# Kernel tuning notes

Hardware: AMD Instinct MI355X
Metric: run time of the kernel (lower is better)

Reference implementation:

```python
import jax, jax.numpy as jnp
import numpy as np

N_NODES = 50000
N_EDGES = 800000
IN_F, HID_F, OUT_F = 256, 128, 64


def setup_inputs() -> dict:
    key = jax.random.key(0)
    ks = jax.random.split(key, 9)
    glorot = lambda k, shp: jax.random.normal(k, shp, jnp.float32) * np.sqrt(2.0 / (shp[0] + shp[1]))
    return {
        "x": jax.random.normal(ks[0], (N_NODES, IN_F), jnp.float32),
        "W1": glorot(ks[1], (IN_F, HID_F)),
        "b1": jnp.zeros((HID_F,), jnp.float32),
        "W2": glorot(ks[2], (HID_F, OUT_F)),
        "b2": jnp.zeros((OUT_F,), jnp.float32),
        "Wf": glorot(ks[3], (OUT_F, 2)),
        "bf": jnp.zeros((2,), jnp.float32),
        "src": jax.random.randint(ks[4], (N_EDGES,), 0, N_NODES, jnp.int32),
        "dst": jax.random.randint(ks[5], (N_EDGES,), 0, N_NODES, jnp.int32),
    }


def _gcn_layer(x, src, dst, W, b):
    # DGL GraphConv, norm='both': h = D_in^{-1/2} A D_out^{-1/2} (x W) + b
    n = x.shape[0]
    ones = jnp.ones((src.shape[0],), x.dtype)
    deg_out = jnp.clip(jax.ops.segment_sum(ones, src, num_segments=n), 1.0)
    deg_in = jnp.clip(jax.ops.segment_sum(ones, dst, num_segments=n), 1.0)
    h = x @ W  # transform first (in_feats >= out_feats), cheaper messages
    h = h * jax.lax.rsqrt(deg_out)[:, None]
    agg = jax.ops.segment_sum(h[src], dst, num_segments=n)  # [N, F] sparse aggregate
    return agg * jax.lax.rsqrt(deg_in)[:, None] + b


def reference(x, W1, b1, W2, b2, Wf, bf, src, dst):
    h1 = jax.nn.relu(_gcn_layer(x, src, dst, W1, b1))
    hidden = _gcn_layer(h1, src, dst, W2, b2)
    logits = hidden @ Wf + bf
    return (logits, hidden)
```

## Files before the change

### kernel.cpp

```cpp
#include <hip/hip_runtime.h>
#include <hip/hip_bf16.h>
#include <cstdint>
#include <cstddef>

#define NNODES 50000
#define NEDGES 800000
#define DHB    64
#define DHC    12500
#define CHUNK1 4096
#define GA1    196
#define GH1TOT (256 * GA1)
#define C2     1000
#define SCB    800
#define GH2TOT (256 * SCB)
#define NBE    ((NEDGES + 255) / 256)

typedef unsigned short u16;
typedef unsigned int u32;
typedef short bfrag8 __attribute__((ext_vector_type(8)));
typedef float f32x4 __attribute__((ext_vector_type(4)));

__device__ __forceinline__ u16 f2bf(float f) {
    union { float f; uint32_t i; } v; v.f = f;
    uint32_t r = (v.i + 0x7FFFu + ((v.i >> 16) & 1u)) >> 16;
    return (u16)r;
}
__device__ __forceinline__ float bflo(u32 p) { union { uint32_t i; float f; } v; v.i = p << 16; return v.f; }
__device__ __forceinline__ float bfhi(u32 p) { union { uint32_t i; float f; } v; v.i = p & 0xFFFF0000u; return v.f; }

__global__ __launch_bounds__(256) void pre_kernel(const float* __restrict__ W1, const float* __restrict__ W2,
                                                  u16* __restrict__ P1, u16* __restrict__ P2,
                                                  const int* __restrict__ src, const int* __restrict__ dst,
                                                  u32* __restrict__ histg, u32* __restrict__ gh1, int nE) {
    __shared__ u32 hh[NNODES / 2];
    int b = blockIdx.x;
    if (b < DHB) {
        for (int j = threadIdx.x; j < NNODES / 2; j += 256) hh[j] = 0;
        __syncthreads();
        int beg = b * DHC, end = min(beg + DHC, nE);
        for (int i = beg + threadIdx.x; i < end; i += 256) {
            u32 n = (u32)src[i];
            atomicAdd(&hh[n >> 1], 1u << ((n & 1) * 16));
        }
        __syncthreads();
        u32* out = histg + (size_t)b * (NNODES / 2);
        for (int j = threadIdx.x; j < NNODES / 2; j += 256) out[j] = hh[j];
    } else if (b < DHB + GA1) {
        int bb = b - DHB;
        hh[threadIdx.x] = 0;
        __syncthreads();
        int beg = bb * CHUNK1, end = min(beg + CHUNK1, nE);
        for (int i = beg + threadIdx.x; i < end; i += 256)
            atomicAdd(&hh[(u32)dst[i] & 255u], 1);
        __syncthreads();
        gh1[threadIdx.x * GA1 + bb] = hh[threadIdx.x];
    } else {
        int i = (b - DHB - GA1) * 256 + threadIdx.x;
        if (i < 256 * 128) {
            int k = i >> 7, n = i & 127;
            P1[((((k >> 3) << 7) + n) << 3) | (k & 7)] = f2bf(W1[i]);
        }
        if (i < 128 * 64) {
            int k = i >> 6, n = i & 63;
            P2[((((k >> 3) << 6) + n) << 3) | (k & 7)] = f2bf(W2[i]);
        }
    }
}

__global__ __launch_bounds__(256) void red_scan1(const u16* __restrict__ histg16, int* __restrict__ deg,
                                                 const u32* __restrict__ gh1, int* __restrict__ scanned,
                                                 int* __restrict__ partials) {
    int i = blockIdx.x * 256 + threadIdx.x;
    if (i < NNODES) {
        int s = 0;
        #pragma unroll 4
        for (int b = 0; b < DHB; b++) s += histg16[(size_t)b * NNODES + i];
        deg[i] = s;
    }
    __shared__ int sd[256];
    int t = threadIdx.x;
    int gi = blockIdx.x * 256 + t;
    int v = (int)gh1[gi];
    sd[t] = v;
    __syncthreads();
    #pragma unroll
    for (int o = 1; o < 256; o <<= 1) {
        int add = (t >= o) ? sd[t - o] : 0;
        __syncthreads();
        sd[t] += add;
        __syncthreads();
    }
    scanned[gi] = sd[t];
    if (t == 255) partials[blockIdx.x] = sd[255];
}

__global__ __launch_bounds__(256) void scatter1(const int* __restrict__ dst, const int* __restrict__ src,
                                                const u32* __restrict__ gh1, const int* __restrict__ scanned,
                                                const int* __restrict__ partials, u32* __restrict__ sbuf, int nE) {
    __shared__ int sd[256];
    __shared__ int offs_l[256];
    __shared__ u32 base[256];
    __shared__ u32 lh[256];
    int t = threadIdx.x;
    int v = (t < GA1) ? partials[t] : 0;
    sd[t] = v;
    __syncthreads();
    #pragma unroll
    for (int o = 1; o < 256; o <<= 1) {
        int add = (t >= o) ? sd[t - o] : 0;
        __syncthreads();
        sd[t] += add;
        __syncthreads();
    }
    offs_l[t] = sd[t] - v;
    __syncthreads();
    int idx = t * GA1 + blockIdx.x;
    base[t] = (u32)(scanned[idx] + offs_l[idx >> 8] - (int)gh1[idx]);
    lh[t] = 0;
    __syncthreads();
    int beg = blockIdx.x * CHUNK1, end = min(beg + CHUNK1, nE);
    for (int i = beg + t; i < end; i += 256) {
        u32 el = ((u32)dst[i] << 16) | (u32)src[i];
        u32 d = (el >> 16) & 255u;
        u32 r = atomicAdd(&lh[d], 1);
        sbuf[base[d] + r] = el;
    }
}

__global__ __launch_bounds__(256) void hist2(const u32* __restrict__ sbuf, u32* __restrict__ gh2, int nE) {
    __shared__ u32 hist[4][256];
    int wave = threadIdx.x >> 6, lane = threadIdx.x & 63;
    int cg = blockIdx.x * 4 + wave;
    for (int j = lane; j < 256; j += 64) hist[wave][j] = 0;
    __syncthreads();
    int beg = cg * C2, end = min(beg + C2, nE);
    for (int i = beg + lane; i < end; i += 64)
        atomicAdd(&hist[wave][sbuf[i] >> 24], 1);
    __syncthreads();
    for (int j = lane; j < 256; j += 64)
        gh2[j * SCB + cg] = hist[wave][j];
}

__global__ __launch_bounds__(256) void scan2(const u32* __restrict__ gh2, int* __restrict__ scanned,
                                             int* __restrict__ partials) {
    __shared__ int sd[256];
    int t = threadIdx.x;
    int gi = blockIdx.x * 256 + t;
    int v = (int)gh2[gi];
    sd[t] = v;
    __syncthreads();
    #pragma unroll
    for (int o = 1; o < 256; o <<= 1) {
        int add = (t >= o) ? sd[t - o] : 0;
        __syncthreads();
        sd[t] += add;
        __syncthreads();
    }
    scanned[gi] = sd[t];
    if (t == 255) partials[blockIdx.x] = sd[255];
}

__global__ __launch_bounds__(256) void scatter2_stable(const u32* __restrict__ sbuf, const u32* __restrict__ gh2,
                                                       const int* __restrict__ scanned, const int* __restrict__ partials,
                                                       u32* __restrict__ sorted, int nE) {
    __shared__ int sd[256];
    __shared__ int offs_l[800];
    __shared__ u32 run[4][256];
    int t = threadIdx.x;
    int v[4]; int s = 0;
    #pragma unroll
    for (int j = 0; j < 4; j++) { int idx = t * 4 + j; v[j] = (idx < 800) ? partials[idx] : 0; s += v[j]; }
    sd[t] = s;
    __syncthreads();
    #pragma unroll
    for (int o = 1; o < 256; o <<= 1) {
        int add = (t >= o) ? sd[t - o] : 0;
        __syncthreads();
        sd[t] += add;
        __syncthreads();
    }
    int bse = sd[t] - s;
    #pragma unroll
    for (int j = 0; j < 4; j++) { int idx = t * 4 + j; if (idx < 800) offs_l[idx] = bse; bse += v[j]; }
    __syncthreads();
    int wave = t >> 6, lane = t & 63;
    int cg = blockIdx.x * 4 + wave;
    for (int j = lane; j < 256; j += 64) {
        int idx = j * SCB + cg;
        run[wave][j] = (u32)(scanned[idx] + offs_l[idx >> 8] - (int)gh2[idx]);
    }
    __syncthreads();
    int beg = cg * C2, end = min(beg + C2, nE);
    for (int i0 = beg; i0 < end; i0 += 64) {
        int i = i0 + lane;
        int active = (i < end);
        u32 el = active ? sbuf[i] : 0;
        u32 d = el >> 24;
        unsigned long long m = __ballot(active);
        #pragma unroll
        for (int b = 0; b < 8; b++) {
            unsigned long long bb_ = __ballot(active && ((d >> b) & 1));
            m &= ((d >> b) & 1) ? bb_ : ~bb_;
        }
        if (active) {
            int lanerank = __popcll(m & ((1ull << lane) - 1ull));
            int leader = __ffsll((long long)m) - 1;
            u32 base = 0;
            if (lane == leader) base = atomicAdd(&run[wave][d], (u32)__popcll(m));
            base = (u32)__shfl((int)base, leader, 64);
            sorted[base + (u32)lanerank] = el;
        }
    }
}

__global__ __launch_bounds__(256) void bounds_kernel(const u32* __restrict__ sorted, int* __restrict__ rp, int nE) {
    int e = blockIdx.x * 256 + threadIdx.x;
    if (e >= nE) return;
    int k = (int)(sorted[e] >> 16);
    int kp = e ? (int)(sorted[e - 1] >> 16) : -1;
    if (k != kp)
        for (int n = kp + 1; n <= k; n++) rp[n] = e;
    if (e == nE - 1)
        for (int n = k + 1; n <= NNODES; n++) rp[n] = nE;
}


template <int K, int N, bool AF32>
__global__ __launch_bounds__(256) void gemm_scaled(const void* __restrict__ A_, const u16* __restrict__ Wp,
                                                   const int* __restrict__ deg, u16* __restrict__ out, int M) {
    const int lane = threadIdx.x & 63;
    const int wave = threadIdx.x >> 6;
    const int m = lane & 15;
    const int q = lane >> 4;
    const int row0 = blockIdx.x * 64 + wave * 16;

    int rowa = row0 + m; if (rowa > M - 1) rowa = M - 1;

    constexpr int NT = N / 16;
    f32x4 acc[NT];
    #pragma unroll
    for (int t = 0; t < NT; t++) acc[t] = (f32x4){0.f, 0.f, 0.f, 0.f};

    #pragma unroll
    for (int kc = 0; kc < K; kc += 32) {
        bfrag8 af;
        if constexpr (AF32) {
            const float* ap = (const float*)A_ + (size_t)rowa * K + q * 8 + kc;
            const float4 x0 = *(const float4*)(ap);
            const float4 x1 = *(const float4*)(ap + 4);
            af[0] = (short)f2bf(x0.x); af[1] = (short)f2bf(x0.y);
            af[2] = (short)f2bf(x0.z); af[3] = (short)f2bf(x0.w);
            af[4] = (short)f2bf(x1.x); af[5] = (short)f2bf(x1.y);
            af[6] = (short)f2bf(x1.z); af[7] = (short)f2bf(x1.w);
        } else {
            const u16* ap = (const u16*)A_ + (size_t)rowa * K + q * 8 + kc;
            af = *(const bfrag8*)ap;
        }
        const u16* bbase = Wp + ((size_t)(((kc >> 3) + q) * N) + m) * 8;
        #pragma unroll
        for (int t = 0; t < NT; t++) {
            bfrag8 bf_ = *(const bfrag8*)(bbase + t * 128);
            acc[t] = __builtin_amdgcn_mfma_f32_16x16x32_bf16(af, bf_, acc[t], 0, 0, 0);
        }
    }
    #pragma unroll
    for (int r = 0; r < 4; r++) {
        int gr = row0 + q * 4 + r;
        if (gr < M) {
            int dO = deg[gr]; if (dO < 1) dO = 1;
            float s = rsqrtf((float)dO);
            #pragma unroll
            for (int t = 0; t < NT; t++)
                out[(size_t)gr * N + t * 16 + m] = f2bf(acc[t][r] * s);
        }
    }
}

__global__ __launch_bounds__(256) void gather1(const uint4* __restrict__ h,
                                               const int* __restrict__ row_ptr,
                                               const u32* __restrict__ sorted, const float* __restrict__ b1,
                                               uint4* __restrict__ h1out, int nNodes) {
    int node = (blockIdx.x * 256 + threadIdx.x) >> 4;
    int l = threadIdx.x & 15;
    if (node >= nNodes) return;
    int beg = row_ptr[node], end = row_ptr[node + 1];
    float a[8] = {0.f, 0.f, 0.f, 0.f, 0.f, 0.f, 0.f, 0.f};
    for (int e = beg; e < end; e += 4) {
        uint4 p[4];
        #pragma unroll
        for (int j = 0; j < 4; j++) {
            int ee = e + j; ee = (ee < end - 1) ? ee : end - 1;
            p[j] = h[(size_t)(sorted[ee] & 0xFFFFu) * 16 + l];
        }
        #pragma unroll
        for (int j = 0; j < 4; j++)
            if (e + j < end) {
                a[0] += bflo(p[j].x); a[1] += bfhi(p[j].x);
                a[2] += bflo(p[j].y); a[3] += bfhi(p[j].y);
                a[4] += bflo(p[j].z); a[5] += bfhi(p[j].z);
                a[6] += bflo(p[j].w); a[7] += bfhi(p[j].w);
            }
    }
    int dI = end - beg; if (dI < 1) dI = 1;
    float r = rsqrtf((float)dI);
    const float4 bA = *(const float4*)(b1 + 8 * l);
    const float4 bB = *(const float4*)(b1 + 8 * l + 4);
    float v0 = fmaxf(a[0] * r + bA.x, 0.f), v1 = fmaxf(a[1] * r + bA.y, 0.f);
    float v2 = fmaxf(a[2] * r + bA.z, 0.f), v3 = fmaxf(a[3] * r + bA.w, 0.f);
    float v4 = fmaxf(a[4] * r + bB.x, 0.f), v5 = fmaxf(a[5] * r + bB.y, 0.f);
    float v6 = fmaxf(a[6] * r + bB.z, 0.f), v7 = fmaxf(a[7] * r + bB.w, 0.f);
    uint4 o;
    o.x = ((u32)f2bf(v1) << 16) | f2bf(v0);
    o.y = ((u32)f2bf(v3) << 16) | f2bf(v2);
    o.z = ((u32)f2bf(v5) << 16) | f2bf(v4);
    o.w = ((u32)f2bf(v7) << 16) | f2bf(v6);
    h1out[(size_t)node * 16 + l] = o;
}

__global__ __launch_bounds__(256) void gather2(const uint4* __restrict__ h2,
                                               const int* __restrict__ row_ptr,
                                               const u32* __restrict__ sorted, const float* __restrict__ b2,
                                               const float* __restrict__ Wf, const float* __restrict__ bfv,
                                               float* __restrict__ logits, float* __restrict__ hidden, int nNodes) {
    int node = (blockIdx.x * 256 + threadIdx.x) >> 3;
    int l = threadIdx.x & 7;
    if (node >= nNodes) return;
    int beg = row_ptr[node], end = row_ptr[node + 1];
    float a[8] = {0.f, 0.f, 0.f, 0.f, 0.f, 0.f, 0.f, 0.f};
    for (int e = beg; e < end; e += 4) {
        uint4 p[4];
        #pragma unroll
        for (int j = 0; j < 4; j++) {
            int ee = e + j; ee = (ee < end - 1) ? ee : end - 1;
            p[j] = h2[(size_t)(sorted[ee] & 0xFFFFu) * 8 + l];
        }
        #pragma unroll
        for (int j = 0; j < 4; j++)
            if (e + j < end) {
                a[0] += bflo(p[j].x); a[1] += bfhi(p[j].x);
                a[2] += bflo(p[j].y); a[3] += bfhi(p[j].y);
                a[4] += bflo(p[j].z); a[5] += bfhi(p[j].z);
                a[6] += bflo(p[j].w); a[7] += bfhi(p[j].w);
            }
    }
    int dI = end - beg; if (dI < 1) dI = 1;
    float r = rsqrtf((float)dI);
    float v[8];
    #pragma unroll
    for (int f = 0; f < 8; f++) v[f] = a[f] * r + b2[8 * l + f];
    float4 oA = {v[0], v[1], v[2], v[3]};
    float4 oB = {v[4], v[5], v[6], v[7]};
    ((float4*)hidden)[(size_t)node * 16 + 2 * l + 0] = oA;
    ((float4*)hidden)[(size_t)node * 16 + 2 * l + 1] = oB;
    float l0 = 0.f, l1 = 0.f;
    #pragma unroll
    for (int f = 0; f < 8; f++) {
        l0 += v[f] * Wf[(8 * l + f) * 2 + 0];
        l1 += v[f] * Wf[(8 * l + f) * 2 + 1];
    }
    #pragma unroll
    for (int off = 4; off > 0; off >>= 1) {
        l0 += __shfl_down(l0, off, 8);
        l1 += __shfl_down(l1, off, 8);
    }
    if (l == 0) {
        logits[(size_t)node * 2 + 0] = l0 + bfv[0];
        logits[(size_t)node * 2 + 1] = l1 + bfv[1];
    }
}

extern "C" void kernel_launch(void* const* d_in, const int* in_sizes, int n_in,
                              void* d_out, int out_size, void* d_ws, size_t ws_size,
                              hipStream_t stream) {
    const float* x   = (const float*)d_in[0];
    const float* W1  = (const float*)d_in[1];
    const float* b1  = (const float*)d_in[2];
    const float* W2  = (const float*)d_in[3];
    const float* b2  = (const float*)d_in[4];
    const float* Wf  = (const float*)d_in[5];
    const float* bfv = (const float*)d_in[6];
    const int* src = (const int*)d_in[7];
    const int* dst = (const int*)d_in[8];

    float* out_logits = (float*)d_out;
    float* out_hidden = (float*)d_out + 2 * NNODES;

    char* ws = (char*)d_ws;
    size_t off = 0;
    auto alloc = [&](size_t bytes) { void* p = ws + off; off += (bytes + 255) & ~(size_t)255; return p; };
    u32*   gh1     = (u32*)alloc(GH1TOT * 4);
    u32*   gh2     = (u32*)alloc(GH2TOT * 4);
    int*   scanned = (int*)alloc(GH2TOT * 4);
    int*   partials= (int*)alloc(1024 * 4);
    u32*   sbuf    = (u32*)alloc((size_t)NEDGES * 4);
    u32*   sorted  = (u32*)alloc((size_t)NEDGES * 4);
    u32*   histg   = (u32*)alloc((size_t)DHB * (NNODES / 2) * 4);
    int*   deg_out = (int*)alloc(NNODES * 4);
    int*   row_ptr = (int*)alloc((NNODES + 1) * 4);
    u16*   Wp1     = (u16*)alloc(256 * 128 * 2);
    u16*   Wp2     = (u16*)alloc(128 * 64 * 2);
    u16*   h       = (u16*)alloc((size_t)NNODES * 128 * 2);
    u16*   h1      = (u16*)alloc((size_t)NNODES * 128 * 2);
    u16*   h2      = (u16*)alloc((size_t)NNODES * 64 * 2);

    pre_kernel<<<DHB + GA1 + 128, 256, 0, stream>>>(W1, W2, Wp1, Wp2, src, dst, histg, gh1, NEDGES);
    red_scan1<<<GA1, 256, 0, stream>>>((const u16*)histg, deg_out, gh1, scanned, partials);
    scatter1<<<GA1, 256, 0, stream>>>(dst, src, gh1, scanned, partials, sbuf, NEDGES);
    hist2<<<SCB / 4, 256, 0, stream>>>(sbuf, gh2, NEDGES);
    scan2<<<GH2TOT / 256, 256, 0, stream>>>(gh2, scanned, partials);
    scatter2_stable<<<SCB / 4, 256, 0, stream>>>(sbuf, gh2, scanned, partials, sorted, NEDGES);
    bounds_kernel<<<NBE, 256, 0, stream>>>(sorted, row_ptr, NEDGES);
    gemm_scaled<256, 128, true><<<(NNODES + 63) / 64, 256, 0, stream>>>(x, Wp1, deg_out, h, NNODES);
    gather1<<<(NNODES * 16 + 255) / 256, 256, 0, stream>>>((const uint4*)h, row_ptr, sorted, b1,
                                                           (uint4*)h1, NNODES);
    gemm_scaled<128, 64, false><<<(NNODES + 63) / 64, 256, 0, stream>>>(h1, Wp2, deg_out, h2, NNODES);
    gather2<<<(NNODES * 8 + 255) / 256, 256, 0, stream>>>((const uint4*)h2, row_ptr, sorted, b2, Wf, bfv,
                                                          out_logits, out_hidden, NNODES);
}
```

Before: 234.3 us.

## Fuse graph-building kernels into one cooperative kernel with grid syncs

The degree histogram, two-pass radix sort by destination, scans and row-pointer construction were seven separate kernel launches. They are merged into a single cooperative kernel of 256 blocks that uses grid.sync() between phases, with chunk sizes retuned to fit the fixed grid. This removes per-launch overhead and the gaps between small dependent kernels. In exchange, each phase is limited to 256 blocks with large shared memory, which lowers parallelism and occupancy, and grid-wide barriers have their own cost.

New measurement: 444.5 us. +89.7%, slower.

```diff
diff --git a/kernel.cpp b/kernel.cpp
--- a/kernel.cpp
+++ b/kernel.cpp
@@ -1,19 +1,22 @@
 #include <hip/hip_runtime.h>
 #include <hip/hip_bf16.h>
+#include <hip/hip_cooperative_groups.h>
 #include <cstdint>
 #include <cstddef>
 
+namespace cg = cooperative_groups;
+
 #define NNODES 50000
 #define NEDGES 800000
+#define NB     256
 #define DHB    64
 #define DHC    12500
-#define CHUNK1 4096
-#define GA1    196
+#define GA1    192
+#define CHUNK1 4167
 #define GH1TOT (256 * GA1)
-#define C2     1000
-#define SCB    800
-#define GH2TOT (256 * SCB)
-#define NBE    ((NEDGES + 255) / 256)
+#define SCB2   1024
+#define C2     782
+#define GH2TOT (256 * SCB2)
 
 typedef unsigned short u16;
 typedef unsigned int u32;
@@ -28,200 +31,206 @@
 __device__ __forceinline__ float bflo(u32 p) { union { uint32_t i; float f; } v; v.i = p << 16; return v.f; }
 __device__ __forceinline__ float bfhi(u32 p) { union { uint32_t i; float f; } v; v.i = p & 0xFFFF0000u; return v.f; }
 
-__global__ __launch_bounds__(256) void pre_kernel(const float* __restrict__ W1, const float* __restrict__ W2,
-                                                  u16* __restrict__ P1, u16* __restrict__ P2,
-                                                  const int* __restrict__ src, const int* __restrict__ dst,
-                                                  u32* __restrict__ histg, u32* __restrict__ gh1, int nE) {
-    __shared__ u32 hh[NNODES / 2];
-    int b = blockIdx.x;
+__global__ void build_graph(const float* __restrict__ W1, const float* __restrict__ W2,
+                            u16* __restrict__ P1w, u16* __restrict__ P2w,
+                            const int* __restrict__ src, const int* __restrict__ dst,
+                            u32* __restrict__ histg, u32* __restrict__ gh1,
+                            int* __restrict__ scan1, int* __restrict__ part1,
+                            u32* __restrict__ sbuf, u32* __restrict__ gh2,
+                            int* __restrict__ scan2g, int* __restrict__ part2,
+                            u32* __restrict__ sorted, int* __restrict__ deg,
+                            int* __restrict__ rp, int nE) {
+    __shared__ __align__(16) u32 ls[25088];
+    cg::grid_group grid = cg::this_grid();
+    const int b = blockIdx.x, t = threadIdx.x;
+
     if (b < DHB) {
-        for (int j = threadIdx.x; j < NNODES / 2; j += 256) hh[j] = 0;
+        for (int j = t; j < NNODES / 2; j += 256) ls[j] = 0;
         __syncthreads();
         int beg = b * DHC, end = min(beg + DHC, nE);
-        for (int i = beg + threadIdx.x; i < end; i += 256) {
+        for (int i = beg + t; i < end; i += 256) {
             u32 n = (u32)src[i];
-            atomicAdd(&hh[n >> 1], 1u << ((n & 1) * 16));
+            atomicAdd(&ls[n >> 1], 1u << ((n & 1) * 16));
         }
         __syncthreads();
         u32* out = histg + (size_t)b * (NNODES / 2);
-        for (int j = threadIdx.x; j < NNODES / 2; j += 256) out[j] = hh[j];
-    } else if (b < DHB + GA1) {
-        int bb = b - DHB;
-        hh[threadIdx.x] = 0;
-        __syncthreads();
-        int beg = bb * CHUNK1, end = min(beg + CHUNK1, nE);
-        for (int i = beg + threadIdx.x; i < end; i += 256)
-            atomicAdd(&hh[(u32)dst[i] & 255u], 1);
-        __syncthreads();
-        gh1[threadIdx.x * GA1 + bb] = hh[threadIdx.x];
+        for (int j = t; j < NNODES / 2; j += 256) out[j] = ls[j];
     } else {
-        int i = (b - DHB - GA1) * 256 + threadIdx.x;
-        if (i < 256 * 128) {
+        int c = b - DHB;
+        ls[t] = 0;
+        __syncthreads();
+        int beg = c * CHUNK1, end = min(beg + CHUNK1, nE);
+        for (int i = beg + t; i < end; i += 256)
+            atomicAdd(&ls[(u32)dst[i] & 255u], 1);
+        __syncthreads();
+        gh1[t * GA1 + c] = ls[t];
+        if (b < 192) {
+            int i = (b - 64) * 256 + t;
             int k = i >> 7, n = i & 127;
-            P1[((((k >> 3) << 7) + n) << 3) | (k & 7)] = f2bf(W1[i]);
-        }
-        if (i < 128 * 64) {
+            P1w[((((k >> 3) << 7) + n) << 3) | (k & 7)] = f2bf(W1[i]);
+        } else if (b < 224) {
+            int i = (b - 192) * 256 + t;
             int k = i >> 6, n = i & 63;
-            P2[((((k >> 3) << 6) + n) << 3) | (k & 7)] = f2bf(W2[i]);
-        }
-    }
-}
-
-__global__ __launch_bounds__(256) void red_scan1(const u16* __restrict__ histg16, int* __restrict__ deg,
-                                                 const u32* __restrict__ gh1, int* __restrict__ scanned,
-                                                 int* __restrict__ partials) {
-    int i = blockIdx.x * 256 + threadIdx.x;
-    if (i < NNODES) {
-        int s = 0;
-        #pragma unroll 4
-        for (int b = 0; b < DHB; b++) s += histg16[(size_t)b * NNODES + i];
-        deg[i] = s;
-    }
-    __shared__ int sd[256];
-    int t = threadIdx.x;
-    int gi = blockIdx.x * 256 + t;
-    int v = (int)gh1[gi];
-    sd[t] = v;
-    __syncthreads();
-    #pragma unroll
-    for (int o = 1; o < 256; o <<= 1) {
-        int add = (t >= o) ? sd[t - o] : 0;
-        __syncthreads();
-        sd[t] += add;
-        __syncthreads();
-    }
-    scanned[gi] = sd[t];
-    if (t == 255) partials[blockIdx.x] = sd[255];
-}
-
-__global__ __launch_bounds__(256) void scatter1(const int* __restrict__ dst, const int* __restrict__ src,
-                                                const u32* __restrict__ gh1, const int* __restrict__ scanned,
-                                                const int* __restrict__ partials, u32* __restrict__ sbuf, int nE) {
-    __shared__ int sd[256];
-    __shared__ int offs_l[256];
-    __shared__ u32 base[256];
-    __shared__ u32 lh[256];
-    int t = threadIdx.x;
-    int v = (t < GA1) ? partials[t] : 0;
-    sd[t] = v;
-    __syncthreads();
-    #pragma unroll
-    for (int o = 1; o < 256; o <<= 1) {
-        int add = (t >= o) ? sd[t - o] : 0;
-        __syncthreads();
-        sd[t] += add;
-        __syncthreads();
-    }
-    offs_l[t] = sd[t] - v;
-    __syncthreads();
-    int idx = t * GA1 + blockIdx.x;
-    base[t] = (u32)(scanned[idx] + offs_l[idx >> 8] - (int)gh1[idx]);
-    lh[t] = 0;
-    __syncthreads();
-    int beg = blockIdx.x * CHUNK1, end = min(beg + CHUNK1, nE);
-    for (int i = beg + t; i < end; i += 256) {
-        u32 el = ((u32)dst[i] << 16) | (u32)src[i];
-        u32 d = (el >> 16) & 255u;
-        u32 r = atomicAdd(&lh[d], 1);
-        sbuf[base[d] + r] = el;
-    }
-}
-
-__global__ __launch_bounds__(256) void hist2(const u32* __restrict__ sbuf, u32* __restrict__ gh2, int nE) {
-    __shared__ u32 hist[4][256];
-    int wave = threadIdx.x >> 6, lane = threadIdx.x & 63;
-    int cg = blockIdx.x * 4 + wave;
-    for (int j = lane; j < 256; j += 64) hist[wave][j] = 0;
-    __syncthreads();
-    int beg = cg * C2, end = min(beg + C2, nE);
-    for (int i = beg + lane; i < end; i += 64)
-        atomicAdd(&hist[wave][sbuf[i] >> 24], 1);
-    __syncthreads();
-    for (int j = lane; j < 256; j += 64)
-        gh2[j * SCB + cg] = hist[wave][j];
-}
-
-__global__ __launch_bounds__(256) void scan2(const u32* __restrict__ gh2, int* __restrict__ scanned,
-                                             int* __restrict__ partials) {
-    __shared__ int sd[256];
-    int t = threadIdx.x;
-    int gi = blockIdx.x * 256 + t;
-    int v = (int)gh2[gi];
-    sd[t] = v;
-    __syncthreads();
-    #pragma unroll
-    for (int o = 1; o < 256; o <<= 1) {
-        int add = (t >= o) ? sd[t - o] : 0;
-        __syncthreads();
-        sd[t] += add;
-        __syncthreads();
-    }
-    scanned[gi] = sd[t];
-    if (t == 255) partials[blockIdx.x] = sd[255];
-}
-
-__global__ __launch_bounds__(256) void scatter2_stable(const u32* __restrict__ sbuf, const u32* __restrict__ gh2,
-                                                       const int* __restrict__ scanned, const int* __restrict__ partials,
-                                                       u32* __restrict__ sorted, int nE) {
-    __shared__ int sd[256];
-    __shared__ int offs_l[800];
-    __shared__ u32 run[4][256];
-    int t = threadIdx.x;
-    int v[4]; int s = 0;
-    #pragma unroll
-    for (int j = 0; j < 4; j++) { int idx = t * 4 + j; v[j] = (idx < 800) ? partials[idx] : 0; s += v[j]; }
-    sd[t] = s;
-    __syncthreads();
-    #pragma unroll
-    for (int o = 1; o < 256; o <<= 1) {
-        int add = (t >= o) ? sd[t - o] : 0;
-        __syncthreads();
-        sd[t] += add;
-        __syncthreads();
-    }
-    int bse = sd[t] - s;
-    #pragma unroll
-    for (int j = 0; j < 4; j++) { int idx = t * 4 + j; if (idx < 800) offs_l[idx] = bse; bse += v[j]; }
-    __syncthreads();
-    int wave = t >> 6, lane = t & 63;
-    int cg = blockIdx.x * 4 + wave;
-    for (int j = lane; j < 256; j += 64) {
-        int idx = j * SCB + cg;
-        run[wave][j] = (u32)(scanned[idx] + offs_l[idx >> 8] - (int)gh2[idx]);
-    }
-    __syncthreads();
-    int beg = cg * C2, end = min(beg + C2, nE);
-    for (int i0 = beg; i0 < end; i0 += 64) {
-        int i = i0 + lane;
-        int active = (i < end);
-        u32 el = active ? sbuf[i] : 0;
-        u32 d = el >> 24;
-        unsigned long long m = __ballot(active);
-        #pragma unroll
-        for (int b = 0; b < 8; b++) {
-            unsigned long long bb_ = __ballot(active && ((d >> b) & 1));
-            m &= ((d >> b) & 1) ? bb_ : ~bb_;
-        }
-        if (active) {
-            int lanerank = __popcll(m & ((1ull << lane) - 1ull));
-            int leader = __ffsll((long long)m) - 1;
-            u32 base = 0;
-            if (lane == leader) base = atomicAdd(&run[wave][d], (u32)__popcll(m));
-            base = (u32)__shfl((int)base, leader, 64);
-            sorted[base + (u32)lanerank] = el;
-        }
-    }
-}
-
-__global__ __launch_bounds__(256) void bounds_kernel(const u32* __restrict__ sorted, int* __restrict__ rp, int nE) {
-    int e = blockIdx.x * 256 + threadIdx.x;
-    if (e >= nE) return;
-    int k = (int)(sorted[e] >> 16);
-    int kp = e ? (int)(sorted[e - 1] >> 16) : -1;
-    if (k != kp)
-        for (int n = kp + 1; n <= k; n++) rp[n] = e;
-    if (e == nE - 1)
-        for (int n = k + 1; n <= NNODES; n++) rp[n] = nE;
+            P2w[((((k >> 3) << 6) + n) << 3) | (k & 7)] = f2bf(W2[i]);
+        }
+    }
+    grid.sync();
+
+    if (b < GA1) {
+        int* sd = (int*)ls;
+        int gi = b * 256 + t;
+        int v = (int)gh1[gi];
+        sd[t] = v;
+        __syncthreads();
+        #pragma unroll
+        for (int o = 1; o < 256; o <<= 1) {
+            int add = (t >= o) ? sd[t - o] : 0;
+            __syncthreads();
+            sd[t] += add;
+            __syncthreads();
+        }
+        scan1[gi] = sd[t];
+        if (t == 255) part1[b] = sd[255];
+    }
+    {
+        int n = b * 196 + t;
+        if (t < 196 && n < NNODES) {
+            int s = 0;
+            #pragma unroll 4
+            for (int bb = 0; bb < DHB; bb++)
+                s += (int)((histg[(size_t)bb * (NNODES / 2) + (n >> 1)] >> ((n & 1) * 16)) & 0xFFFFu);
+            deg[n] = s;
+        }
+    }
+    grid.sync();
+
+    if (b >= DHB) {
+        int c = b - DHB;
+        int* sd    = (int*)ls;
+        int* offsL = (int*)(ls + 256);
+        u32* baseL = ls + 512;
+        u32* lh    = ls + 768;
+        int v = (t < GA1) ? part1[t] : 0;
+        sd[t] = v;
+        __syncthreads();
+        #pragma unroll
+        for (int o = 1; o < 256; o <<= 1) {
+            int add = (t >= o) ? sd[t - o] : 0;
+            __syncthreads();
+            sd[t] += add;
+            __syncthreads();
+        }
+        if (t < GA1) offsL[t] = sd[t] - v;
+        __syncthreads();
+        int idx = t * GA1 + c;
+        baseL[t] = (u32)(scan1[idx] + offsL[idx >> 8] - (int)gh1[idx]);
+        lh[t] = 0;
+        __syncthreads();
+        int beg = c * CHUNK1, end = min(beg + CHUNK1, nE);
+        for (int i = beg + t; i < end; i += 256) {
+            u32 el = ((u32)dst[i] << 16) | (u32)src[i];
+            u32 d = (el >> 16) & 255u;
+            u32 r = atomicAdd(&lh[d], 1);
+            sbuf[baseL[d] + r] = el;
+        }
+    }
+    grid.sync();
+
+    {
+        int w = t >> 6, lane = t & 63;
+        int cgi = b * 4 + w;
+        for (int j = lane; j < 256; j += 64) ls[w * 256 + j] = 0;
+        __syncthreads();
+        int beg = cgi * C2, end = min(beg + C2, nE);
+        for (int i = beg + lane; i < end; i += 64)
+            atomicAdd(&ls[w * 256 + (sbuf[i] >> 24)], 1);
+        __syncthreads();
+        for (int j = lane; j < 256; j += 64)
+            gh2[j * SCB2 + cgi] = ls[w * 256 + j];
+    }
+    grid.sync();
+
+    {
+        int* sd = (int*)ls;
+        for (int gg = 0; gg < 4; gg++) {
+            int g = b * 4 + gg;
+            int gi = g * 256 + t;
+            int v = (int)gh2[gi];
+            sd[t] = v;
+            __syncthreads();
+            #pragma unroll
+            for (int o = 1; o < 256; o <<= 1) {
+                int add = (t >= o) ? sd[t - o] : 0;
+                __syncthreads();
+                sd[t] += add;
+                __syncthreads();
+            }
+            scan2g[gi] = sd[t];
+            if (t == 255) part2[g] = sd[255];
+            __syncthreads();
+        }
+    }
+    grid.sync();
+
+    {
+        int* sd    = (int*)ls;
+        int* offs2 = (int*)(ls + 256);
+        u32* run   = ls + 1280;
+        int v4[4]; int s = 0;
+        #pragma unroll
+        for (int j = 0; j < 4; j++) { v4[j] = part2[t * 4 + j]; s += v4[j]; }
+        sd[t] = s;
+        __syncthreads();
+        #pragma unroll
+        for (int o = 1; o < 256; o <<= 1) {
+            int add = (t >= o) ? sd[t - o] : 0;
+            __syncthreads();
+            sd[t] += add;
+            __syncthreads();
+        }
+        int bse = sd[t] - s;
+        #pragma unroll
+        for (int j = 0; j < 4; j++) { offs2[t * 4 + j] = bse; bse += v4[j]; }
+        __syncthreads();
+        int w = t >> 6, lane = t & 63;
+        int cgi = b * 4 + w;
+        for (int j = lane; j < 256; j += 64) {
+            int idx = j * SCB2 + cgi;
+            run[w * 256 + j] = (u32)(scan2g[idx] + offs2[idx >> 8] - (int)gh2[idx]);
+        }
+        __syncthreads();
+        int beg = cgi * C2, end = min(beg + C2, nE);
+        for (int i0 = beg; i0 < end; i0 += 64) {
+            int i = i0 + lane;
+            int active = (i < end);
+            u32 el = active ? sbuf[i] : 0;
+            u32 d = el >> 24;
+            unsigned long long m = __ballot(active);
+            #pragma unroll
+            for (int bb = 0; bb < 8; bb++) {
+                unsigned long long bm = __ballot(active && ((d >> bb) & 1));
+                m &= ((d >> bb) & 1) ? bm : ~bm;
+            }
+            if (active) {
+                int lanerank = __popcll(m & ((1ull << lane) - 1ull));
+                int leader = __ffsll((long long)m) - 1;
+                u32 base = 0;
+                if (lane == leader) base = atomicAdd(&run[w * 256 + d], (u32)__popcll(m));
+                base = (u32)__shfl((int)base, leader, 64);
+                sorted[base + (u32)lanerank] = el;
+            }
+        }
+    }
+    grid.sync();
+
+    for (int e = b * 256 + t; e < nE; e += NB * 256) {
+        int k = (int)(sorted[e] >> 16);
+        int kp = e ? (int)(sorted[e - 1] >> 16) : -1;
+        if (k != kp)
+            for (int n = kp + 1; n <= k; n++) rp[n] = e;
+        if (e == nE - 1)
+            for (int n = k + 1; n <= NNODES; n++) rp[n] = nE;
+    }
 }
 
 
@@ -276,8 +285,7 @@
     }
 }
 
-__global__ __launch_bounds__(256) void gather1(const uint4* __restrict__ h,
-                                               const int* __restrict__ row_ptr,
+__global__ __launch_bounds__(256) void gather1(const uint4* __restrict__ h, const int* __restrict__ row_ptr,
                                                const u32* __restrict__ sorted, const float* __restrict__ b1,
                                                uint4* __restrict__ h1out, int nNodes) {
     int node = (blockIdx.x * 256 + threadIdx.x) >> 4;
@@ -317,8 +325,7 @@
     h1out[(size_t)node * 16 + l] = o;
 }
 
-__global__ __launch_bounds__(256) void gather2(const uint4* __restrict__ h2,
-                                               const int* __restrict__ row_ptr,
+__global__ __launch_bounds__(256) void gather2(const uint4* __restrict__ h2, const int* __restrict__ row_ptr,
                                                const u32* __restrict__ sorted, const float* __restrict__ b2,
                                                const float* __restrict__ Wf, const float* __restrict__ bfv,
                                                float* __restrict__ logits, float* __restrict__ hidden, int nNodes) {
@@ -390,8 +397,10 @@
     auto alloc = [&](size_t bytes) { void* p = ws + off; off += (bytes + 255) & ~(size_t)255; return p; };
     u32*   gh1     = (u32*)alloc(GH1TOT * 4);
     u32*   gh2     = (u32*)alloc(GH2TOT * 4);
-    int*   scanned = (int*)alloc(GH2TOT * 4);
-    int*   partials= (int*)alloc(1024 * 4);
+    int*   scan1   = (int*)alloc(GH1TOT * 4);
+    int*   scan2g  = (int*)alloc(GH2TOT * 4);
+    int*   part1   = (int*)alloc(256 * 4);
+    int*   part2   = (int*)alloc(1024 * 4);
     u32*   sbuf    = (u32*)alloc((size_t)NEDGES * 4);
     u32*   sorted  = (u32*)alloc((size_t)NEDGES * 4);
     u32*   histg   = (u32*)alloc((size_t)DHB * (NNODES / 2) * 4);
@@ -403,13 +412,13 @@
     u16*   h1      = (u16*)alloc((size_t)NNODES * 128 * 2);
     u16*   h2      = (u16*)alloc((size_t)NNODES * 64 * 2);
 
-    pre_kernel<<<DHB + GA1 + 128, 256, 0, stream>>>(W1, W2, Wp1, Wp2, src, dst, histg, gh1, NEDGES);
-    red_scan1<<<GA1, 256, 0, stream>>>((const u16*)histg, deg_out, gh1, scanned, partials);
-    scatter1<<<GA1, 256, 0, stream>>>(dst, src, gh1, scanned, partials, sbuf, NEDGES);
-    hist2<<<SCB / 4, 256, 0, stream>>>(sbuf, gh2, NEDGES);
-    scan2<<<GH2TOT / 256, 256, 0, stream>>>(gh2, scanned, partials);
-    scatter2_stable<<<SCB / 4, 256, 0, stream>>>(sbuf, gh2, scanned, partials, sorted, NEDGES);
-    bounds_kernel<<<NBE, 256, 0, stream>>>(sorted, row_ptr, NEDGES);
+    int nE = NEDGES;
+    void* kargs[] = { (void*)&W1, (void*)&W2, (void*)&Wp1, (void*)&Wp2, (void*)&src, (void*)&dst,
+                      (void*)&histg, (void*)&gh1, (void*)&scan1, (void*)&part1, (void*)&sbuf,
+                      (void*)&gh2, (void*)&scan2g, (void*)&part2, (void*)&sorted,
+                      (void*)&deg_out, (void*)&row_ptr, (void*)&nE };
+    hipLaunchCooperativeKernel((void*)build_graph, dim3(NB), dim3(256), kargs, 0, stream);
+
     gemm_scaled<256, 128, true><<<(NNODES + 63) / 64, 256, 0, stream>>>(x, Wp1, deg_out, h, NNODES);
     gather1<<<(NNODES * 16 + 255) / 256, 256, 0, stream>>>((const uint4*)h, row_ptr, sorted, b1,
                                                            (uint4*)h1, NNODES);
```

## Replace two-pass LSD radix sort with MSD bucket partition plus per-bucket local sort

Applied to the files above, without the earlier changes.

The edge sort by destination switches from a low-byte-then-high-byte LSD radix (hist2, scan2, a stable ballot scatter, and a bounds kernel) to an MSD scheme. Edges are first partitioned by dst>>8 into 196 buckets over 256 chunks. Each bucket is then sorted by the low byte in a single block that also writes row_ptr directly. This removes three kernel launches and a full pass over the edges. Order within a node becomes nondeterministic because of the atomics, so float summation order can vary between runs. The gather loops also unroll to 8 loads in flight.

Result: faster. 217.2 us (-7.3%).

```diff
diff --git a/kernel.cpp b/kernel.cpp
--- a/kernel.cpp
+++ b/kernel.cpp
@@ -7,13 +7,9 @@
 #define NEDGES 800000
 #define DHB    64
 #define DHC    12500
-#define CHUNK1 4096
-#define GA1    196
-#define GH1TOT (256 * GA1)
-#define C2     1000
-#define SCB    800
-#define GH2TOT (256 * SCB)
-#define NBE    ((NEDGES + 255) / 256)
+#define NCH    256
+#define CHUNK1 3125
+#define NBUCK  196
 
 typedef unsigned short u16;
 typedef unsigned int u32;
@@ -33,29 +29,29 @@
                                                   const int* __restrict__ src, const int* __restrict__ dst,
                                                   u32* __restrict__ histg, u32* __restrict__ gh1, int nE) {
     __shared__ u32 hh[NNODES / 2];
-    int b = blockIdx.x;
+    int b = blockIdx.x, t = threadIdx.x;
     if (b < DHB) {
-        for (int j = threadIdx.x; j < NNODES / 2; j += 256) hh[j] = 0;
+        for (int j = t; j < NNODES / 2; j += 256) hh[j] = 0;
         __syncthreads();
         int beg = b * DHC, end = min(beg + DHC, nE);
-        for (int i = beg + threadIdx.x; i < end; i += 256) {
+        for (int i = beg + t; i < end; i += 256) {
             u32 n = (u32)src[i];
             atomicAdd(&hh[n >> 1], 1u << ((n & 1) * 16));
         }
         __syncthreads();
         u32* out = histg + (size_t)b * (NNODES / 2);
-        for (int j = threadIdx.x; j < NNODES / 2; j += 256) out[j] = hh[j];
-    } else if (b < DHB + GA1) {
-        int bb = b - DHB;
-        hh[threadIdx.x] = 0;
-        __syncthreads();
-        int beg = bb * CHUNK1, end = min(beg + CHUNK1, nE);
-        for (int i = beg + threadIdx.x; i < end; i += 256)
-            atomicAdd(&hh[(u32)dst[i] & 255u], 1);
-        __syncthreads();
-        gh1[threadIdx.x * GA1 + bb] = hh[threadIdx.x];
+        for (int j = t; j < NNODES / 2; j += 256) out[j] = hh[j];
+    } else if (b < DHB + NCH) {
+        int c = b - DHB;
+        hh[t] = 0;
+        __syncthreads();
+        int beg = c * CHUNK1, end = min(beg + CHUNK1, nE);
+        for (int i = beg + t; i < end; i += 256)
+            atomicAdd(&hh[(u32)dst[i] >> 8], 1);
+        __syncthreads();
+        gh1[t * NCH + c] = hh[t];
     } else {
-        int i = (b - DHB - GA1) * 256 + threadIdx.x;
+        int i = (b - DHB - NCH) * 256 + t;
         if (i < 256 * 128) {
             int k = i >> 7, n = i & 127;
             P1[((((k >> 3) << 7) + n) << 3) | (k & 7)] = f2bf(W1[i]);
@@ -67,19 +63,20 @@
     }
 }
 
-__global__ __launch_bounds__(256) void red_scan1(const u16* __restrict__ histg16, int* __restrict__ deg,
-                                                 const u32* __restrict__ gh1, int* __restrict__ scanned,
-                                                 int* __restrict__ partials) {
-    int i = blockIdx.x * 256 + threadIdx.x;
-    if (i < NNODES) {
+__global__ __launch_bounds__(256) void red_scan1(const u32* __restrict__ histg, int* __restrict__ deg,
+                                                 const u32* __restrict__ gh1, int* __restrict__ scan1,
+                                                 int* __restrict__ part1) {
+    int t = threadIdx.x, b = blockIdx.x;
+    int n = b * 196 + t;
+    if (t < 196 && n < NNODES) {
         int s = 0;
         #pragma unroll 4
-        for (int b = 0; b < DHB; b++) s += histg16[(size_t)b * NNODES + i];
-        deg[i] = s;
+        for (int bb = 0; bb < DHB; bb++)
+            s += (int)((histg[(size_t)bb * (NNODES / 2) + (n >> 1)] >> ((n & 1) * 16)) & 0xFFFFu);
+        deg[n] = s;
     }
     __shared__ int sd[256];
-    int t = threadIdx.x;
-    int gi = blockIdx.x * 256 + t;
+    int gi = b * NCH + t;
     int v = (int)gh1[gi];
     sd[t] = v;
     __syncthreads();
@@ -90,19 +87,19 @@
         sd[t] += add;
         __syncthreads();
     }
-    scanned[gi] = sd[t];
-    if (t == 255) partials[blockIdx.x] = sd[255];
+    scan1[gi] = sd[t];
+    if (t == 255) part1[b] = sd[255];
 }
 
 __global__ __launch_bounds__(256) void scatter1(const int* __restrict__ dst, const int* __restrict__ src,
-                                                const u32* __restrict__ gh1, const int* __restrict__ scanned,
-                                                const int* __restrict__ partials, u32* __restrict__ sbuf, int nE) {
+                                                const u32* __restrict__ gh1, const int* __restrict__ scan1,
+                                                const int* __restrict__ part1, u32* __restrict__ sbuf, int nE) {
     __shared__ int sd[256];
-    __shared__ int offs_l[256];
+    __shared__ int offs[256];
     __shared__ u32 base[256];
     __shared__ u32 lh[256];
-    int t = threadIdx.x;
-    int v = (t < GA1) ? partials[t] : 0;
+    int t = threadIdx.x, c = blockIdx.x;
+    int v = part1[t];
     sd[t] = v;
     __syncthreads();
     #pragma unroll
@@ -112,41 +109,27 @@
         sd[t] += add;
         __syncthreads();
     }
-    offs_l[t] = sd[t] - v;
-    __syncthreads();
-    int idx = t * GA1 + blockIdx.x;
-    base[t] = (u32)(scanned[idx] + offs_l[idx >> 8] - (int)gh1[idx]);
+    offs[t] = sd[t] - v;
+    __syncthreads();
+    base[t] = (u32)(scan1[t * NCH + c] + offs[t] - (int)gh1[t * NCH + c]);
     lh[t] = 0;
     __syncthreads();
-    int beg = blockIdx.x * CHUNK1, end = min(beg + CHUNK1, nE);
+    int beg = c * CHUNK1, end = min(beg + CHUNK1, nE);
     for (int i = beg + t; i < end; i += 256) {
         u32 el = ((u32)dst[i] << 16) | (u32)src[i];
-        u32 d = (el >> 16) & 255u;
+        u32 d = el >> 24;
         u32 r = atomicAdd(&lh[d], 1);
         sbuf[base[d] + r] = el;
     }
 }
 
-__global__ __launch_bounds__(256) void hist2(const u32* __restrict__ sbuf, u32* __restrict__ gh2, int nE) {
-    __shared__ u32 hist[4][256];
-    int wave = threadIdx.x >> 6, lane = threadIdx.x & 63;
-    int cg = blockIdx.x * 4 + wave;
-    for (int j = lane; j < 256; j += 64) hist[wave][j] = 0;
-    __syncthreads();
-    int beg = cg * C2, end = min(beg + C2, nE);
-    for (int i = beg + lane; i < end; i += 64)
-        atomicAdd(&hist[wave][sbuf[i] >> 24], 1);
-    __syncthreads();
-    for (int j = lane; j < 256; j += 64)
-        gh2[j * SCB + cg] = hist[wave][j];
-}
-
-__global__ __launch_bounds__(256) void scan2(const u32* __restrict__ gh2, int* __restrict__ scanned,
-                                             int* __restrict__ partials) {
+__global__ __launch_bounds__(256) void sort_bucket(const u32* __restrict__ sbuf, const int* __restrict__ part1,
+                                                   u32* __restrict__ sorted, int* __restrict__ rp, int nE) {
     __shared__ int sd[256];
-    int t = threadIdx.x;
-    int gi = blockIdx.x * 256 + t;
-    int v = (int)gh2[gi];
+    __shared__ int cnt[256];
+    __shared__ int cursor[256];
+    int t = threadIdx.x, b = blockIdx.x;
+    int v = part1[t];
     sd[t] = v;
     __syncthreads();
     #pragma unroll
@@ -156,21 +139,17 @@
         sd[t] += add;
         __syncthreads();
     }
-    scanned[gi] = sd[t];
-    if (t == 255) partials[blockIdx.x] = sd[255];
-}
-
-__global__ __launch_bounds__(256) void scatter2_stable(const u32* __restrict__ sbuf, const u32* __restrict__ gh2,
-                                                       const int* __restrict__ scanned, const int* __restrict__ partials,
-                                                       u32* __restrict__ sorted, int nE) {
-    __shared__ int sd[256];
-    __shared__ int offs_l[800];
-    __shared__ u32 run[4][256];
-    int t = threadIdx.x;
-    int v[4]; int s = 0;
-    #pragma unroll
-    for (int j = 0; j < 4; j++) { int idx = t * 4 + j; v[j] = (idx < 800) ? partials[idx] : 0; s += v[j]; }
-    sd[t] = s;
+    __shared__ int bs_s, bl_s;
+    if (t == b) { bs_s = sd[t] - v; bl_s = v; }
+    __syncthreads();
+    int bstart = bs_s, bend = bstart + bl_s;
+    cnt[t] = 0;
+    __syncthreads();
+    for (int i = bstart + t; i < bend; i += 256)
+        atomicAdd(&cnt[(sbuf[i] >> 16) & 255u], 1);
+    __syncthreads();
+    int cv = cnt[t];
+    sd[t] = cv;
     __syncthreads();
     #pragma unroll
     for (int o = 1; o < 256; o <<= 1) {
@@ -179,49 +158,17 @@
         sd[t] += add;
         __syncthreads();
     }
-    int bse = sd[t] - s;
-    #pragma unroll
-    for (int j = 0; j < 4; j++) { int idx = t * 4 + j; if (idx < 800) offs_l[idx] = bse; bse += v[j]; }
-    __syncthreads();
-    int wave = t >> 6, lane = t & 63;
-    int cg = blockIdx.x * 4 + wave;
-    for (int j = lane; j < 256; j += 64) {
-        int idx = j * SCB + cg;
-        run[wave][j] = (u32)(scanned[idx] + offs_l[idx >> 8] - (int)gh2[idx]);
-    }
-    __syncthreads();
-    int beg = cg * C2, end = min(beg + C2, nE);
-    for (int i0 = beg; i0 < end; i0 += 64) {
-        int i = i0 + lane;
-        int active = (i < end);
-        u32 el = active ? sbuf[i] : 0;
-        u32 d = el >> 24;
-        unsigned long long m = __ballot(active);
-        #pragma unroll
-        for (int b = 0; b < 8; b++) {
-            unsigned long long bb_ = __ballot(active && ((d >> b) & 1));
-            m &= ((d >> b) & 1) ? bb_ : ~bb_;
-        }
-        if (active) {
-            int lanerank = __popcll(m & ((1ull << lane) - 1ull));
-            int leader = __ffsll((long long)m) - 1;
-            u32 base = 0;
-            if (lane == leader) base = atomicAdd(&run[wave][d], (u32)__popcll(m));
-            base = (u32)__shfl((int)base, leader, 64);
-            sorted[base + (u32)lanerank] = el;
-        }
-    }
-}
-
-__global__ __launch_bounds__(256) void bounds_kernel(const u32* __restrict__ sorted, int* __restrict__ rp, int nE) {
-    int e = blockIdx.x * 256 + threadIdx.x;
-    if (e >= nE) return;
-    int k = (int)(sorted[e] >> 16);
-    int kp = e ? (int)(sorted[e - 1] >> 16) : -1;
-    if (k != kp)
-        for (int n = kp + 1; n <= k; n++) rp[n] = e;
-    if (e == nE - 1)
-        for (int n = k + 1; n <= NNODES; n++) rp[n] = nE;
+    int excl = sd[t] - cv;
+    int node = b * 256 + t;
+    if (node < NNODES) rp[node] = bstart + excl;
+    if (b == NBUCK - 1 && t == 0) rp[NNODES] = nE;
+    cursor[t] = excl;
+    __syncthreads();
+    for (int i = bstart + t; i < bend; i += 256) {
+        u32 el = sbuf[i];
+        int r = atomicAdd(&cursor[(el >> 16) & 255u], 1);
+        sorted[bstart + r] = el;
+    }
 }
 
 
@@ -276,8 +223,7 @@
     }
 }
 
-__global__ __launch_bounds__(256) void gather1(const uint4* __restrict__ h,
-                                               const int* __restrict__ row_ptr,
+__global__ __launch_bounds__(256) void gather1(const uint4* __restrict__ h, const int* __restrict__ row_ptr,
                                                const u32* __restrict__ sorted, const float* __restrict__ b1,
                                                uint4* __restrict__ h1out, int nNodes) {
     int node = (blockIdx.x * 256 + threadIdx.x) >> 4;
@@ -285,15 +231,15 @@
     if (node >= nNodes) return;
     int beg = row_ptr[node], end = row_ptr[node + 1];
     float a[8] = {0.f, 0.f, 0.f, 0.f, 0.f, 0.f, 0.f, 0.f};
-    for (int e = beg; e < end; e += 4) {
-        uint4 p[4];
-        #pragma unroll
-        for (int j = 0; j < 4; j++) {
+    for (int e = beg; e < end; e += 8) {
+        uint4 p[8];
+        #pragma unroll
+        for (int j = 0; j < 8; j++) {
             int ee = e + j; ee = (ee < end - 1) ? ee : end - 1;
             p[j] = h[(size_t)(sorted[ee] & 0xFFFFu) * 16 + l];
         }
         #pragma unroll
-        for (int j = 0; j < 4; j++)
+        for (int j = 0; j < 8; j++)
             if (e + j < end) {
                 a[0] += bflo(p[j].x); a[1] += bfhi(p[j].x);
                 a[2] += bflo(p[j].y); a[3] += bfhi(p[j].y);
@@ -317,8 +263,7 @@
     h1out[(size_t)node * 16 + l] = o;
 }
 
-__global__ __launch_bounds__(256) void gather2(const uint4* __restrict__ h2,
-                                               const int* __restrict__ row_ptr,
+__global__ __launch_bounds__(256) void gather2(const uint4* __restrict__ h2, const int* __restrict__ row_ptr,
                                                const u32* __restrict__ sorted, const float* __restrict__ b2,
                                                const float* __restrict__ Wf, const float* __restrict__ bfv,
                                                float* __restrict__ logits, float* __restrict__ hidden, int nNodes) {
@@ -327,15 +272,15 @@
     if (node >= nNodes) return;
     int beg = row_ptr[node], end = row_ptr[node + 1];
     float a[8] = {0.f, 0.f, 0.f, 0.f, 0.f, 0.f, 0.f, 0.f};
-    for (int e = beg; e < end; e += 4) {
-        uint4 p[4];
-        #pragma unroll
-        for (int j = 0; j < 4; j++) {
+    for (int e = beg; e < end; e += 8) {
+        uint4 p[8];
+        #pragma unroll
+        for (int j = 0; j < 8; j++) {
             int ee = e + j; ee = (ee < end - 1) ? ee : end - 1;
             p[j] = h2[(size_t)(sorted[ee] & 0xFFFFu) * 8 + l];
         }
         #pragma unroll
-        for (int j = 0; j < 4; j++)
+        for (int j = 0; j < 8; j++)
             if (e + j < end) {
                 a[0] += bflo(p[j].x); a[1] += bfhi(p[j].x);
                 a[2] += bflo(p[j].y); a[3] += bfhi(p[j].y);
@@ -388,10 +333,9 @@
     char* ws = (char*)d_ws;
     size_t off = 0;
     auto alloc = [&](size_t bytes) { void* p = ws + off; off += (bytes + 255) & ~(size_t)255; return p; };
-    u32*   gh1     = (u32*)alloc(GH1TOT * 4);
-    u32*   gh2     = (u32*)alloc(GH2TOT * 4);
-    int*   scanned = (int*)alloc(GH2TOT * 4);
-    int*   partials= (int*)alloc(1024 * 4);
+    u32*   gh1     = (u32*)alloc(NCH * NCH * 4);
+    int*   scan1   = (int*)alloc(NCH * NCH * 4);
+    int*   part1   = (int*)alloc(256 * 4);
     u32*   sbuf    = (u32*)alloc((size_t)NEDGES * 4);
     u32*   sorted  = (u32*)alloc((size_t)NEDGES * 4);
     u32*   histg   = (u32*)alloc((size_t)DHB * (NNODES / 2) * 4);
@@ -403,13 +347,10 @@
     u16*   h1      = (u16*)alloc((size_t)NNODES * 128 * 2);
     u16*   h2      = (u16*)alloc((size_t)NNODES * 64 * 2);
 
-    pre_kernel<<<DHB + GA1 + 128, 256, 0, stream>>>(W1, W2, Wp1, Wp2, src, dst, histg, gh1, NEDGES);
-    red_scan1<<<GA1, 256, 0, stream>>>((const u16*)histg, deg_out, gh1, scanned, partials);
-    scatter1<<<GA1, 256, 0, stream>>>(dst, src, gh1, scanned, partials, sbuf, NEDGES);
-    hist2<<<SCB / 4, 256, 0, stream>>>(sbuf, gh2, NEDGES);
-    scan2<<<GH2TOT / 256, 256, 0, stream>>>(gh2, scanned, partials);
-    scatter2_stable<<<SCB / 4, 256, 0, stream>>>(sbuf, gh2, scanned, partials, sorted, NEDGES);
-    bounds_kernel<<<NBE, 256, 0, stream>>>(sorted, row_ptr, NEDGES);
+    pre_kernel<<<DHB + NCH + 128, 256, 0, stream>>>(W1, W2, Wp1, Wp2, src, dst, histg, gh1, NEDGES);
+    red_scan1<<<NCH, 256, 0, stream>>>(histg, deg_out, gh1, scan1, part1);
+    scatter1<<<NCH, 256, 0, stream>>>(dst, src, gh1, scan1, part1, sbuf, NEDGES);
+    sort_bucket<<<NBUCK, 256, 0, stream>>>(sbuf, part1, sorted, row_ptr, NEDGES);
     gemm_scaled<256, 128, true><<<(NNODES + 63) / 64, 256, 0, stream>>>(x, Wp1, deg_out, h, NNODES);
     gather1<<<(NNODES * 16 + 255) / 256, 256, 0, stream>>>((const uint4*)h, row_ptr, sorted, b1,
                                                            (uint4*)h1, NNODES);
```
